# Optimization experiments

Measured on AMD Instinct MI355X. Metric: run time of the kernel, lower is better.

Reference implementation:

```python
import jax, jax.numpy as jnp
import numpy as np

LN_EPS = 1e-5


def setup_inputs() -> dict:
    key = jax.random.key(0)
    ks = jax.random.split(key, 5)
    B, S, DIN, DOUT = 4, 2048, 4096, 4096
    return {
        "x": jax.random.normal(ks[0], (B, S, DIN), dtype=jnp.float32),
        "weight": jax.random.normal(ks[1], (DOUT, DIN), dtype=jnp.float32),
        "in_channel_scale": jax.random.uniform(ks[2], (DIN,), dtype=jnp.float32, minval=0.1, maxval=1.0),
        "out_channel_scale": jax.random.uniform(ks[3], (DOUT,), dtype=jnp.float32, minval=0.1, maxval=1.0),
        "bias": jax.random.normal(ks[4], (DOUT,), dtype=jnp.float32) * 0.02,
        "ln_gamma": jnp.ones((DOUT,), dtype=jnp.float32),
        "ln_beta": jnp.zeros((DOUT,), dtype=jnp.float32),
    }


def reference(x, weight, in_channel_scale, out_channel_scale, bias, ln_gamma, ln_beta):
    # BitNet-style 1-bit quantization of the weight (sign), per-channel scaling.
    w_bin = jnp.sign(weight)  # [out, in], values in {-1, 0, +1}
    # (x * in_scale) @ w_bin.T * out_scale + bias
    h = jnp.einsum('bsi,oi->bso', x * in_channel_scale, w_bin) * out_channel_scale + bias
    # LayerNorm over out_features with learnable affine
    mu = jnp.mean(h, axis=-1, keepdims=True)
    var = jnp.mean(jnp.square(h - mu), axis=-1, keepdims=True)
    h = (h - mu) * jax.lax.rsqrt(var + LN_EPS)
    return h * ln_gamma + ln_beta
```

## Files before the change

### kernel.cpp

```cpp
#include <hip/hip_runtime.h>
#include <hip/hip_bf16.h>

constexpr int GM = 8192;
constexpr int GN = 4096;
constexpr int GK = 4096;

constexpr int BM = 256, BN = 256, BK = 64;
constexpr int NSTEP = GK / BK;
constexpr int SLOT_BYTES = (BM + BN) * BK;
constexpr int LDS_BYTES = 3 * SLOT_BYTES;

using bf16x8 = __attribute__((ext_vector_type(8))) __bf16;
using i32x4  = __attribute__((ext_vector_type(4))) int;

__global__ __launch_bounds__(256) void prep_x_i8(
    const float* __restrict__ x, const float* __restrict__ iscale,
    signed char* __restrict__ A, float* __restrict__ alpha) {
  int row = blockIdx.x;
  const float* xr = x + (size_t)row * GK;
  int t = threadIdx.x;

  float v[16];
  float mx = 0.f;
#pragma unroll
  for (int p = 0; p < 4; ++p) {
    int idx = p * 1024 + t * 4;
    float4 xv = *(const float4*)(xr + idx);
    float4 sv = *(const float4*)(iscale + idx);
    float a0 = xv.x * sv.x, a1 = xv.y * sv.y, a2 = xv.z * sv.z, a3 = xv.w * sv.w;
    v[p * 4 + 0] = a0; v[p * 4 + 1] = a1; v[p * 4 + 2] = a2; v[p * 4 + 3] = a3;
    mx = fmaxf(mx, fmaxf(fmaxf(fabsf(a0), fabsf(a1)), fmaxf(fabsf(a2), fabsf(a3))));
  }
#pragma unroll
  for (int off = 32; off > 0; off >>= 1)
    mx = fmaxf(mx, __shfl_down(mx, off));
  __shared__ float rm[4];
  int wid = t >> 6, lane = t & 63;
  if (lane == 0) rm[wid] = mx;
  __syncthreads();
  float m = fmaxf(fmaxf(rm[0], rm[1]), fmaxf(rm[2], rm[3]));
  float inv = m > 0.f ? 127.f / m : 0.f;
  if (t == 0) alpha[row] = m * (1.f / 127.f);

#pragma unroll
  for (int p = 0; p < 4; ++p) {
    int idx = p * 1024 + t * 4;
    char4 q;
    int q0 = (int)rintf(v[p * 4 + 0] * inv);
    int q1 = (int)rintf(v[p * 4 + 1] * inv);
    int q2 = (int)rintf(v[p * 4 + 2] * inv);
    int q3 = (int)rintf(v[p * 4 + 3] * inv);
    q.x = (signed char)max(-127, min(127, q0));
    q.y = (signed char)max(-127, min(127, q1));
    q.z = (signed char)max(-127, min(127, q2));
    q.w = (signed char)max(-127, min(127, q3));
    *(char4*)(A + (size_t)row * GK + idx) = q;
  }
}

__global__ __launch_bounds__(256) void prep_w_i8(
    const float* __restrict__ w, signed char* __restrict__ Wb) {
  int e = (blockIdx.x * 256 + threadIdx.x) * 8;
  float4 v0 = *(const float4*)(w + e);
  float4 v1 = *(const float4*)(w + e + 4);
  auto sg = [](float v) -> signed char {
    return (signed char)((v > 0.f) - (v < 0.f));
  };
  union { signed char c[8]; unsigned long long u; } o;
  o.c[0] = sg(v0.x); o.c[1] = sg(v0.y); o.c[2] = sg(v0.z); o.c[3] = sg(v0.w);
  o.c[4] = sg(v1.x); o.c[5] = sg(v1.y); o.c[6] = sg(v1.z); o.c[7] = sg(v1.w);
  *(unsigned long long*)(Wb + e) = o.u;
}

__device__ inline void gload16(const void* g, const void* l) {
  __builtin_amdgcn_global_load_lds(
      (const __attribute__((address_space(1))) void*)g,
      (__attribute__((address_space(3))) void*)l, 16, 0, 0);
}

__global__ __launch_bounds__(512, 2) void gemm_i8(
    const signed char* __restrict__ A, const signed char* __restrict__ Bm,
    const float* __restrict__ alpha, float* __restrict__ C) {
  extern __shared__ signed char lds8[];

  int bid = blockIdx.x;
  int x = bid & 7, idx = bid >> 3;
  int brow = ((x & 3) << 3) | (idx & 7);
  int bcol = ((x >> 2) << 3) | (idx >> 3);

  int tid = threadIdx.x, wid = tid >> 6, lane = tid & 63;
  int wm = wid & 1, wn = wid >> 1;
  int lrow = lane & 15, lkhi = lane >> 4;

  const signed char* Ab = A + (size_t)(brow * BM) * GK;
  const signed char* Bb = Bm + (size_t)(bcol * BN) * GK;

  int rchunk = lkhi ^ ((lrow >> 1) & 3);
  int avbase = (wm * 128 + lrow) * 64 + rchunk * 16;
  int bvbase = 16384 + (wn * 64 + lrow) * 64 + rchunk * 16;

  int grow = tid >> 2;
  int gcol = ((tid & 3) ^ ((tid >> 3) & 3)) * 16;

  auto STAGE_A = [&](int kstep, int si) {
    const signed char* s = Ab + (size_t)grow * GK + kstep * BK + gcol;
    const signed char* d = lds8 + si * SLOT_BYTES + tid * 16;
    gload16(s, d);
    gload16(s + (size_t)128 * GK, d + 8192);
  };
  auto STAGE_B = [&](int kstep, int si) {
    const signed char* s = Bb + (size_t)grow * GK + kstep * BK + gcol;
    const signed char* d = lds8 + si * SLOT_BYTES + 16384 + tid * 16;
    gload16(s, d);
    gload16(s + (size_t)128 * GK, d + 8192);
  };

  i32x4 acc[8][4] = {};

  STAGE_A(0, 0); STAGE_B(0, 0);
  STAGE_A(1, 1); STAGE_B(1, 1);
  asm volatile("s_waitcnt vmcnt(4)" ::: "memory");
  __builtin_amdgcn_s_barrier();

  int rc = 0, rs = 2;
  for (int t = 0; t < NSTEP; ++t) {
    const signed char* sl = lds8 + rc * SLOT_BYTES;
    i32x4 af[8], bf[4];

#pragma unroll
    for (int mi = 0; mi < 4; ++mi)
      af[mi] = *(const i32x4*)(sl + avbase + mi * 1024);
#pragma unroll
    for (int ni = 0; ni < 4; ++ni)
      bf[ni] = *(const i32x4*)(sl + bvbase + ni * 1024);
    if (t + 2 < NSTEP) STAGE_A(t + 2, rs);
    __builtin_amdgcn_s_barrier();
    asm volatile("s_waitcnt lgkmcnt(0)" ::: "memory");
    __builtin_amdgcn_sched_barrier(0);
    __builtin_amdgcn_s_setprio(1);
#pragma unroll
    for (int mi = 0; mi < 4; ++mi)
#pragma unroll
      for (int ni = 0; ni < 4; ++ni)
        acc[mi][ni] = __builtin_amdgcn_mfma_i32_16x16x64_i8(
            af[mi], bf[ni], acc[mi][ni], 0, 0, 0);
    __builtin_amdgcn_s_setprio(0);
    __builtin_amdgcn_s_barrier();

#pragma unroll
    for (int mi = 0; mi < 4; ++mi)
      af[4 + mi] = *(const i32x4*)(sl + avbase + (4 + mi) * 1024);
    if (t + 2 < NSTEP) STAGE_B(t + 2, rs);
    __builtin_amdgcn_s_barrier();
    asm volatile("s_waitcnt lgkmcnt(0)" ::: "memory");
    __builtin_amdgcn_sched_barrier(0);
    __builtin_amdgcn_s_setprio(1);
#pragma unroll
    for (int mi = 0; mi < 4; ++mi)
#pragma unroll
      for (int ni = 0; ni < 4; ++ni)
        acc[4 + mi][ni] = __builtin_amdgcn_mfma_i32_16x16x64_i8(
            af[4 + mi], bf[ni], acc[4 + mi][ni], 0, 0, 0);
    __builtin_amdgcn_s_setprio(0);
    __builtin_amdgcn_sched_barrier(0);
    if (t + 2 < NSTEP) asm volatile("s_waitcnt vmcnt(4)" ::: "memory");
    else               asm volatile("s_waitcnt vmcnt(0)" ::: "memory");
    __builtin_amdgcn_s_barrier();
    rc = (rc == 2) ? 0 : rc + 1;
    rs = (rs == 2) ? 0 : rs + 1;
  }

  int crow0 = brow * BM + wm * 128;
  int ccol0 = bcol * BN + wn * 64;
  char* Cb = (char*)C;
#pragma unroll
  for (int mi = 0; mi < 8; ++mi)
#pragma unroll
    for (int ni = 0; ni < 4; ++ni) {
      int col = ccol0 + ni * 16 + lrow;
#pragma unroll
      for (int r = 0; r < 4; ++r) {
        int row = crow0 + mi * 16 + lkhi * 4 + r;
        float h = alpha[row] * (float)acc[mi][ni][r];
        *(__bf16*)(Cb + (size_t)row * 16384 + 8192 + col * 2) = (__bf16)h;
      }
    }
}

__global__ __launch_bounds__(256) void ln_fuse(
    float* __restrict__ out, const float* __restrict__ os,
    const float* __restrict__ bs, const float* __restrict__ g,
    const float* __restrict__ be) {
  constexpr int N = GN;
  int row = blockIdx.x;
  const __bf16* hr = (const __bf16*)((const char*)out + (size_t)row * 16384 + 8192);
  float* orow = out + (size_t)row * N;
  int t = threadIdx.x;

  float v[16];
  float sum = 0.f, ssq = 0.f;
#pragma unroll
  for (int c = 0; c < 2; ++c) {
    int idx = c * 2048 + t * 8;
    bf16x8 hv = *(const bf16x8*)(hr + idx);
    float4 s0 = *(const float4*)(os + idx);
    float4 s1 = *(const float4*)(os + idx + 4);
    float4 b0 = *(const float4*)(bs + idx);
    float4 b1 = *(const float4*)(bs + idx + 4);
#pragma unroll
    for (int j = 0; j < 4; ++j) {
      float a = (float)hv[j] * (&s0.x)[j] + (&b0.x)[j];
      v[c * 8 + j] = a;
      sum += a; ssq += a * a;
    }
#pragma unroll
    for (int j = 0; j < 4; ++j) {
      float a = (float)hv[4 + j] * (&s1.x)[j] + (&b1.x)[j];
      v[c * 8 + 4 + j] = a;
      sum += a; ssq += a * a;
    }
  }

#pragma unroll
  for (int off = 32; off > 0; off >>= 1) {
    sum += __shfl_down(sum, off);
    ssq += __shfl_down(ssq, off);
  }
  __shared__ float rs[8];
  int wid = t >> 6, lane = t & 63;
  if (lane == 0) { rs[wid] = sum; rs[4 + wid] = ssq; }
  __syncthreads();
  sum = rs[0] + rs[1] + rs[2] + rs[3];
  ssq = rs[4] + rs[5] + rs[6] + rs[7];

  float mean = sum * (1.f / N);
  float var = ssq * (1.f / N) - mean * mean;
  float rstd = rsqrtf(var + 1e-5f);

#pragma unroll
  for (int c = 0; c < 2; ++c) {
    int idx = c * 2048 + t * 8;
    float4 g0 = *(const float4*)(g + idx);
    float4 g1 = *(const float4*)(g + idx + 4);
    float4 e0 = *(const float4*)(be + idx);
    float4 e1 = *(const float4*)(be + idx + 4);
    float4 o0, o1;
#pragma unroll
    for (int j = 0; j < 4; ++j) {
      (&o0.x)[j] = (v[c * 8 + j] - mean) * rstd * (&g0.x)[j] + (&e0.x)[j];
      (&o1.x)[j] = (v[c * 8 + 4 + j] - mean) * rstd * (&g1.x)[j] + (&e1.x)[j];
    }
    *(float4*)(orow + idx) = o0;
    *(float4*)(orow + idx + 4) = o1;
  }
}

extern "C" void kernel_launch(void* const* d_in, const int* in_sizes, int n_in,
                              void* d_out, int out_size, void* d_ws, size_t ws_size,
                              hipStream_t stream) {
  const float* x      = (const float*)d_in[0];
  const float* w      = (const float*)d_in[1];
  const float* iscale = (const float*)d_in[2];
  const float* oscale = (const float*)d_in[3];
  const float* bias   = (const float*)d_in[4];
  const float* gamma  = (const float*)d_in[5];
  const float* beta   = (const float*)d_in[6];
  float* out = (float*)d_out;

  signed char* Ai8 = (signed char*)d_ws;
  signed char* Wi8 = (signed char*)d_ws + (size_t)GM * GK;
  float* alpha = (float*)((char*)d_ws + (size_t)GM * GK + (size_t)GN * GK);

  (void)hipFuncSetAttribute((const void*)gemm_i8,
                            hipFuncAttributeMaxDynamicSharedMemorySize, LDS_BYTES);

  prep_x_i8<<<GM, 256, 0, stream>>>(x, iscale, Ai8, alpha);
  prep_w_i8<<<(GN * GK) / (256 * 8), 256, 0, stream>>>(w, Wi8);
  gemm_i8<<<(GM / BM) * (GN / BN), 512, LDS_BYTES, stream>>>(Ai8, Wi8, alpha, out);
  ln_fuse<<<GM, 256, 0, stream>>>(out, oscale, bias, gamma, beta);
}
```

Baseline: 219.7 us.

## Fuse prep kernels and switch GEMM to double-buffered LDS pipeline

The x-quantization and weight-sign kernels are merged into one launch that branches on block index, removing a launch and letting the two prep phases share the GPU. The GEMM drops from a three-slot LDS ring with prefetch depth two to a two-slot double buffer. Each step now issues the full A and B tile load for the next step up front and waits on vmcnt(0) at the end of the step. This lowers LDS use per block but shortens the prefetch distance, so global-load latency may be exposed more often.

```diff
diff --git a/kernel.cpp b/kernel.cpp
--- a/kernel.cpp
+++ b/kernel.cpp
@@ -8,68 +8,70 @@
 constexpr int BM = 256, BN = 256, BK = 64;
 constexpr int NSTEP = GK / BK;
 constexpr int SLOT_BYTES = (BM + BN) * BK;
-constexpr int LDS_BYTES = 3 * SLOT_BYTES;
+constexpr int LDS_BYTES = 2 * SLOT_BYTES;
+
+constexpr int PX_BLOCKS = GM;
+constexpr int PW_BLOCKS = (GN * GK) / (256 * 8);
 
 using bf16x8 = __attribute__((ext_vector_type(8))) __bf16;
 using i32x4  = __attribute__((ext_vector_type(4))) int;
 
-__global__ __launch_bounds__(256) void prep_x_i8(
+__global__ __launch_bounds__(256) void prep_fused_i8(
     const float* __restrict__ x, const float* __restrict__ iscale,
-    signed char* __restrict__ A, float* __restrict__ alpha) {
-  int row = blockIdx.x;
-  const float* xr = x + (size_t)row * GK;
+    const float* __restrict__ w, signed char* __restrict__ A,
+    signed char* __restrict__ Wb, float* __restrict__ alpha) {
+  int b = blockIdx.x;
   int t = threadIdx.x;
-
-  float v[16];
-  float mx = 0.f;
-#pragma unroll
-  for (int p = 0; p < 4; ++p) {
-    int idx = p * 1024 + t * 4;
-    float4 xv = *(const float4*)(xr + idx);
-    float4 sv = *(const float4*)(iscale + idx);
-    float a0 = xv.x * sv.x, a1 = xv.y * sv.y, a2 = xv.z * sv.z, a3 = xv.w * sv.w;
-    v[p * 4 + 0] = a0; v[p * 4 + 1] = a1; v[p * 4 + 2] = a2; v[p * 4 + 3] = a3;
-    mx = fmaxf(mx, fmaxf(fmaxf(fabsf(a0), fabsf(a1)), fmaxf(fabsf(a2), fabsf(a3))));
-  }
-#pragma unroll
-  for (int off = 32; off > 0; off >>= 1)
-    mx = fmaxf(mx, __shfl_down(mx, off));
-  __shared__ float rm[4];
-  int wid = t >> 6, lane = t & 63;
-  if (lane == 0) rm[wid] = mx;
-  __syncthreads();
-  float m = fmaxf(fmaxf(rm[0], rm[1]), fmaxf(rm[2], rm[3]));
-  float inv = m > 0.f ? 127.f / m : 0.f;
-  if (t == 0) alpha[row] = m * (1.f / 127.f);
-
-#pragma unroll
-  for (int p = 0; p < 4; ++p) {
-    int idx = p * 1024 + t * 4;
-    char4 q;
-    int q0 = (int)rintf(v[p * 4 + 0] * inv);
-    int q1 = (int)rintf(v[p * 4 + 1] * inv);
-    int q2 = (int)rintf(v[p * 4 + 2] * inv);
-    int q3 = (int)rintf(v[p * 4 + 3] * inv);
-    q.x = (signed char)max(-127, min(127, q0));
-    q.y = (signed char)max(-127, min(127, q1));
-    q.z = (signed char)max(-127, min(127, q2));
-    q.w = (signed char)max(-127, min(127, q3));
-    *(char4*)(A + (size_t)row * GK + idx) = q;
-  }
-}
-
-__global__ __launch_bounds__(256) void prep_w_i8(
-    const float* __restrict__ w, signed char* __restrict__ Wb) {
-  int e = (blockIdx.x * 256 + threadIdx.x) * 8;
-  float4 v0 = *(const float4*)(w + e);
-  float4 v1 = *(const float4*)(w + e + 4);
-  auto sg = [](float v) -> signed char {
-    return (signed char)((v > 0.f) - (v < 0.f));
-  };
-  union { signed char c[8]; unsigned long long u; } o;
-  o.c[0] = sg(v0.x); o.c[1] = sg(v0.y); o.c[2] = sg(v0.z); o.c[3] = sg(v0.w);
-  o.c[4] = sg(v1.x); o.c[5] = sg(v1.y); o.c[6] = sg(v1.z); o.c[7] = sg(v1.w);
-  *(unsigned long long*)(Wb + e) = o.u;
+  if (b < PX_BLOCKS) {
+    int row = b;
+    const float* xr = x + (size_t)row * GK;
+    float v[16];
+    float mx = 0.f;
+#pragma unroll
+    for (int p = 0; p < 4; ++p) {
+      int idx = p * 1024 + t * 4;
+      float4 xv = *(const float4*)(xr + idx);
+      float4 sv = *(const float4*)(iscale + idx);
+      float a0 = xv.x * sv.x, a1 = xv.y * sv.y, a2 = xv.z * sv.z, a3 = xv.w * sv.w;
+      v[p * 4 + 0] = a0; v[p * 4 + 1] = a1; v[p * 4 + 2] = a2; v[p * 4 + 3] = a3;
+      mx = fmaxf(mx, fmaxf(fmaxf(fabsf(a0), fabsf(a1)), fmaxf(fabsf(a2), fabsf(a3))));
+    }
+#pragma unroll
+    for (int off = 32; off > 0; off >>= 1)
+      mx = fmaxf(mx, __shfl_down(mx, off));
+    __shared__ float rm[4];
+    int wid = t >> 6, lane = t & 63;
+    if (lane == 0) rm[wid] = mx;
+    __syncthreads();
+    float m = fmaxf(fmaxf(rm[0], rm[1]), fmaxf(rm[2], rm[3]));
+    float inv = m > 0.f ? 127.f / m : 0.f;
+    if (t == 0) alpha[row] = m * (1.f / 127.f);
+#pragma unroll
+    for (int p = 0; p < 4; ++p) {
+      int idx = p * 1024 + t * 4;
+      char4 q;
+      int q0 = (int)rintf(v[p * 4 + 0] * inv);
+      int q1 = (int)rintf(v[p * 4 + 1] * inv);
+      int q2 = (int)rintf(v[p * 4 + 2] * inv);
+      int q3 = (int)rintf(v[p * 4 + 3] * inv);
+      q.x = (signed char)max(-127, min(127, q0));
+      q.y = (signed char)max(-127, min(127, q1));
+      q.z = (signed char)max(-127, min(127, q2));
+      q.w = (signed char)max(-127, min(127, q3));
+      *(char4*)(A + (size_t)row * GK + idx) = q;
+    }
+  } else {
+    int e = ((b - PX_BLOCKS) * 256 + t) * 8;
+    float4 v0 = *(const float4*)(w + e);
+    float4 v1 = *(const float4*)(w + e + 4);
+    auto sg = [](float v) -> signed char {
+      return (signed char)((v > 0.f) - (v < 0.f));
+    };
+    union { signed char c[8]; unsigned long long u; } o;
+    o.c[0] = sg(v0.x); o.c[1] = sg(v0.y); o.c[2] = sg(v0.z); o.c[3] = sg(v0.w);
+    o.c[4] = sg(v1.x); o.c[5] = sg(v1.y); o.c[6] = sg(v1.z); o.c[7] = sg(v1.w);
+    *(unsigned long long*)(Wb + e) = o.u;
+  }
 }
 
 __device__ inline void gload16(const void* g, const void* l) {
@@ -102,38 +104,33 @@
   int grow = tid >> 2;
   int gcol = ((tid & 3) ^ ((tid >> 3) & 3)) * 16;
 
-  auto STAGE_A = [&](int kstep, int si) {
-    const signed char* s = Ab + (size_t)grow * GK + kstep * BK + gcol;
-    const signed char* d = lds8 + si * SLOT_BYTES + tid * 16;
-    gload16(s, d);
-    gload16(s + (size_t)128 * GK, d + 8192);
+  auto STAGE = [&](int kstep, int si) {
+    const signed char* sA = Ab + (size_t)grow * GK + kstep * BK + gcol;
+    const signed char* dA = lds8 + si * SLOT_BYTES + tid * 16;
+    gload16(sA, dA);
+    gload16(sA + (size_t)128 * GK, dA + 8192);
+    const signed char* sB = Bb + (size_t)grow * GK + kstep * BK + gcol;
+    gload16(sB, dA + 16384);
+    gload16(sB + (size_t)128 * GK, dA + 16384 + 8192);
   };
-  auto STAGE_B = [&](int kstep, int si) {
-    const signed char* s = Bb + (size_t)grow * GK + kstep * BK + gcol;
-    const signed char* d = lds8 + si * SLOT_BYTES + 16384 + tid * 16;
-    gload16(s, d);
-    gload16(s + (size_t)128 * GK, d + 8192);
-  };
 
   i32x4 acc[8][4] = {};
 
-  STAGE_A(0, 0); STAGE_B(0, 0);
-  STAGE_A(1, 1); STAGE_B(1, 1);
-  asm volatile("s_waitcnt vmcnt(4)" ::: "memory");
+  STAGE(0, 0);
+  asm volatile("s_waitcnt vmcnt(0)" ::: "memory");
   __builtin_amdgcn_s_barrier();
 
-  int rc = 0, rs = 2;
   for (int t = 0; t < NSTEP; ++t) {
-    const signed char* sl = lds8 + rc * SLOT_BYTES;
+    const signed char* sl = lds8 + (t & 1) * SLOT_BYTES;
+    if (t + 1 < NSTEP) STAGE(t + 1, (t + 1) & 1);
+
     i32x4 af[8], bf[4];
-
 #pragma unroll
     for (int mi = 0; mi < 4; ++mi)
       af[mi] = *(const i32x4*)(sl + avbase + mi * 1024);
 #pragma unroll
     for (int ni = 0; ni < 4; ++ni)
       bf[ni] = *(const i32x4*)(sl + bvbase + ni * 1024);
-    if (t + 2 < NSTEP) STAGE_A(t + 2, rs);
     __builtin_amdgcn_s_barrier();
     asm volatile("s_waitcnt lgkmcnt(0)" ::: "memory");
     __builtin_amdgcn_sched_barrier(0);
@@ -150,7 +147,6 @@
 #pragma unroll
     for (int mi = 0; mi < 4; ++mi)
       af[4 + mi] = *(const i32x4*)(sl + avbase + (4 + mi) * 1024);
-    if (t + 2 < NSTEP) STAGE_B(t + 2, rs);
     __builtin_amdgcn_s_barrier();
     asm volatile("s_waitcnt lgkmcnt(0)" ::: "memory");
     __builtin_amdgcn_sched_barrier(0);
@@ -162,12 +158,12 @@
         acc[4 + mi][ni] = __builtin_amdgcn_mfma_i32_16x16x64_i8(
             af[4 + mi], bf[ni], acc[4 + mi][ni], 0, 0, 0);
     __builtin_amdgcn_s_setprio(0);
-    __builtin_amdgcn_sched_barrier(0);
-    if (t + 2 < NSTEP) asm volatile("s_waitcnt vmcnt(4)" ::: "memory");
-    else               asm volatile("s_waitcnt vmcnt(0)" ::: "memory");
-    __builtin_amdgcn_s_barrier();
-    rc = (rc == 2) ? 0 : rc + 1;
-    rs = (rs == 2) ? 0 : rs + 1;
+
+    if (t + 1 < NSTEP) {
+      __builtin_amdgcn_sched_barrier(0);
+      asm volatile("s_waitcnt vmcnt(0)" ::: "memory");
+      __builtin_amdgcn_s_barrier();
+    }
   }
 
   int crow0 = brow * BM + wm * 128;
@@ -274,8 +270,8 @@
   (void)hipFuncSetAttribute((const void*)gemm_i8,
                             hipFuncAttributeMaxDynamicSharedMemorySize, LDS_BYTES);
 
-  prep_x_i8<<<GM, 256, 0, stream>>>(x, iscale, Ai8, alpha);
-  prep_w_i8<<<(GN * GK) / (256 * 8), 256, 0, stream>>>(w, Wi8);
+  prep_fused_i8<<<PX_BLOCKS + PW_BLOCKS, 256, 0, stream>>>(x, iscale, w, Ai8,
+                                                           Wi8, alpha);
   gemm_i8<<<(GM / BM) * (GN / BN), 512, LDS_BYTES, stream>>>(Ai8, Wi8, alpha, out);
   ln_fuse<<<GM, 256, 0, stream>>>(out, oscale, bias, gamma, beta);
 }
```

Result: no change. 217.9 us (-0.8%).
